# Kernel tuning notes

Hardware: AMD Instinct MI355X
Metric: run time of the kernel (lower is better)

The kernel has to match this reference:

```python
import jax, jax.numpy as jnp
import numpy as np

B, LQ, D, H, NL, NP, DFF = 8, 1800, 256, 8, 4, 4, 1024
DH = D // H
SHAPES = np.array([[100, 150], [50, 75], [25, 38], [13, 19]], dtype=np.int64)
LIN = int((SHAPES[:, 0] * SHAPES[:, 1]).sum())
QN, QP = -8.0, 7.0  # 4-bit signed LSQ


def lsq(w, alpha):
    """LSQ weight quantization (per-tensor scale, STE round/grad-scale)."""
    g = 1.0 / jnp.sqrt(w.size * QP)
    a = alpha * g + jax.lax.stop_gradient(alpha - alpha * g)  # grad-scaled alpha
    wn = jnp.clip(w / a, QN, QP)
    wq = wn + jax.lax.stop_gradient(jnp.round(wn) - wn)       # round with STE
    return wq * a


def linear_q(x, w, b, a):
    return x @ lsq(w, a).T + b


def layer_norm(x, g, b, eps=1e-5):
    m = x.mean(-1, keepdims=True)
    v = ((x - m) ** 2).mean(-1, keepdims=True)
    return (x - m) / jnp.sqrt(v + eps) * g + b


def setup_inputs():
    key = jax.random.key(0)
    ks = list(jax.random.split(key, 20))

    def nrm(i, shape, s=0.02):
        return jax.random.normal(ks[i], shape, jnp.float32) * s

    def alpha(w):
        return 2.0 * jnp.mean(jnp.abs(w)) / jnp.sqrt(QP)

    qW, kW, vW, oW = nrm(0, (D, D)), nrm(1, (D, D)), nrm(2, (D, D)), nrm(3, (D, D))
    val_W = nrm(4, (D, D))
    off_W = nrm(5, (H * NL * NP * 2, D))
    aw_W = nrm(6, (H * NL * NP, D))
    out_W = nrm(7, (D, D))
    W1, W2 = nrm(8, (DFF, D)), nrm(9, (D, DFF))
    lsi = np.concatenate([[0], np.cumsum(SHAPES[:, 0] * SHAPES[:, 1])[:-1]]).astype(np.int64)
    z = jnp.zeros
    return dict(
        tgt=nrm(10, (B, LQ, D), 1.0),
        query_pos=nrm(11, (B, LQ, D), 1.0),
        reference_points=jax.random.uniform(ks[12], (B, LQ, NL, 2), jnp.float32),
        src=nrm(13, (B, LIN, D), 1.0),
        qW=qW, qb=z(D), kW=kW, kb=z(D), vW=vW, vb=z(D), oW=oW, ob=z(D),
        a_q=alpha(qW), a_k=alpha(kW), a_v=alpha(vW), a_o=alpha(oW),
        val_W=val_W, val_b=z(D), a_val=alpha(val_W),
        off_W=off_W, off_b=z(H * NL * NP * 2),
        aw_W=aw_W, aw_b=z(H * NL * NP),
        out_W=out_W, out_b=z(D), a_out=alpha(out_W),
        W1=W1, b1=z(DFF), a_w1=alpha(W1),
        W2=W2, b2=z(D), a_w2=alpha(W2),
        ln1_g=jnp.ones(D), ln1_b=z(D),
        ln2_g=jnp.ones(D), ln2_b=z(D),
        ln3_g=jnp.ones(D), ln3_b=z(D),
        src_spatial_shapes=jnp.asarray(SHAPES),
        level_start_index=jnp.asarray(lsi),
        src_padding_mask=jnp.zeros((B, LIN), dtype=bool),
    )


def reference(tgt, query_pos, reference_points, src,
              qW, qb, kW, kb, vW, vb, oW, ob, a_q, a_k, a_v, a_o,
              val_W, val_b, a_val, off_W, off_b, aw_W, aw_b, out_W, out_b, a_out,
              W1, b1, a_w1, W2, b2, a_w2,
              ln1_g, ln1_b, ln2_g, ln2_b, ln3_g, ln3_b,
              src_spatial_shapes, level_start_index, src_padding_mask):
    shapes = np.asarray(src_spatial_shapes)  # static spatial shapes per level

    # ---- quantized self-attention (dropout = eval mode, i.e. identity) ----
    qk_in = tgt + query_pos
    q = linear_q(qk_in, qW, qb, a_q).reshape(B, LQ, H, DH)
    k = linear_q(qk_in, kW, kb, a_k).reshape(B, LQ, H, DH)
    v = linear_q(tgt, vW, vb, a_v).reshape(B, LQ, H, DH)
    scores = jnp.einsum('bqhd,bkhd->bhqk', q, k) / jnp.sqrt(jnp.float32(DH))
    p = jax.nn.softmax(scores, axis=-1)
    sa = jnp.einsum('bhqk,bkhd->bqhd', p, v).reshape(B, LQ, D)
    tgt = layer_norm(tgt + linear_q(sa, oW, ob, a_o), ln2_g, ln2_b)

    # ---- quantized multi-scale deformable cross-attention ----
    query = tgt + query_pos
    value = linear_q(src, val_W, val_b, a_val)
    value = jnp.where(src_padding_mask[..., None], 0.0, value)
    value = value.reshape(B, LIN, H, DH)
    offs = (query @ off_W.T + off_b).reshape(B, LQ, H, NL, NP, 2)
    aw = (query @ aw_W.T + aw_b).reshape(B, LQ, H, NL * NP)
    aw = jax.nn.softmax(aw, axis=-1).reshape(B, LQ, H, NL, NP)
    # offset normalizer is (W_l, H_l)
    norm = jnp.asarray(shapes[:, ::-1].astype(np.float32))  # [NL, 2]
    loc = reference_points[:, :, None, :, None, :] + offs / norm[None, None, None, :, None, :]

    bidx = jnp.arange(B)[:, None, None, None]
    hidx = jnp.arange(H)[None, None, :, None]
    acc = jnp.zeros((B, LQ, H, DH), jnp.float32)
    start = 0
    for l in range(NL):
        Hl, Wl = int(shapes[l, 0]), int(shapes[l, 1])
        v_l = jax.lax.dynamic_slice_in_dim(value, start, Hl * Wl, 1).reshape(B, Hl, Wl, H, DH)
        # grid_sample semantics: align_corners=False, zero padding
        x = loc[:, :, :, l, :, 0] * Wl - 0.5  # [B, LQ, H, NP]
        y = loc[:, :, :, l, :, 1] * Hl - 0.5
        x0 = jnp.floor(x); y0 = jnp.floor(y)
        x0i = x0.astype(jnp.int32); y0i = y0.astype(jnp.int32)
        wx1 = x - x0; wy1 = y - y0
        wx0 = 1.0 - wx1; wy0 = 1.0 - wy1

        def gather(yi, xi):
            valid = (yi >= 0) & (yi < Hl) & (xi >= 0) & (xi < Wl)
            yc = jnp.clip(yi, 0, Hl - 1); xc = jnp.clip(xi, 0, Wl - 1)
            g = v_l[bidx, yc, xc, hidx]  # [B, LQ, H, NP, DH]
            return g * valid[..., None]

        samp = (gather(y0i, x0i) * (wy0 * wx0)[..., None]
                + gather(y0i, x0i + 1) * (wy0 * wx1)[..., None]
                + gather(y0i + 1, x0i) * (wy1 * wx0)[..., None]
                + gather(y0i + 1, x0i + 1) * (wy1 * wx1)[..., None])
        acc = acc + (aw[:, :, :, l, :, None] * samp).sum(axis=3)
        start += Hl * Wl

    ca = linear_q(acc.reshape(B, LQ, D), out_W, out_b, a_out)
    tgt = layer_norm(tgt + ca, ln1_g, ln1_b)

    # ---- quantized FFN ----
    t2 = linear_q(jax.nn.relu(linear_q(tgt, W1, b1, a_w1)), W2, b2, a_w2)
    tgt = layer_norm(tgt + t2, ln3_g, ln3_b)
    return tgt
```

## Files before the change

kernel.cpp:

```cpp
#include <hip/hip_runtime.h>
#include <hip/hip_bf16.h>

static constexpr int B_   = 8;
static constexpr int LQ_  = 1800;
static constexpr int D_   = 256;
static constexpr int H_   = 8;
static constexpr int DFF_ = 1024;
static constexpr int LIN_ = 19947;
static constexpr int MQ_  = B_ * LQ_;
static constexpr int NELEM_ = MQ_ * D_;

#define CDIV(a, b) (((a) + (b) - 1) / (b))

typedef unsigned short u16;
typedef unsigned int   u32;
typedef unsigned long long u64;
typedef __attribute__((ext_vector_type(8))) __bf16 bf16x8;
typedef __attribute__((ext_vector_type(4))) float  f32x4;
typedef __attribute__((ext_vector_type(4))) u32    u32x4;

#if __has_builtin(__builtin_amdgcn_exp2f)
#define EXP2(x) __builtin_amdgcn_exp2f(x)
#else
#define EXP2(x) exp2f(x)
#endif

__device__ __forceinline__ u16 f2bf(float f) {
    union { __bf16 h; u16 u; } v; v.h = (__bf16)f; return v.u;
}
__device__ __forceinline__ float bf2f(u16 u) {
    union { u32 u; float f; } v; v.u = ((u32)u) << 16;
    return v.f;
}

__device__ __forceinline__ f32x4 mfma_bf16(bf16x8 a, bf16x8 b, f32x4 c) {
    return __builtin_amdgcn_mfma_f32_16x16x32_bf16(a, b, c, 0, 0, 0);
}

__global__ void k_quant(const float* __restrict__ w, const float* __restrict__ alpha,
                        u16* __restrict__ o, int n) {
    int i = blockIdx.x * blockDim.x + threadIdx.x;
    if (i >= n) return;
    float a = alpha[0];
    float wn = fminf(fmaxf(w[i] / a, -8.f), 7.f);
    o[i] = f2bf(rintf(wn) * a);
}

__global__ void k_cvt(const float* __restrict__ w, u16* __restrict__ o, int n) {
    int i = blockIdx.x * blockDim.x + threadIdx.x;
    if (i < n) o[i] = f2bf(w[i]);
}

__global__ void k_addcvt(const float* __restrict__ a, const float* __restrict__ b,
                         u16* __restrict__ o, int n) {
    int i = blockIdx.x * blockDim.x + threadIdx.x;
    if (i < n) o[i] = f2bf(a[i] + b[i]);
}

__global__ void k_addcvt2(const u16* __restrict__ a, const float* __restrict__ b,
                          u16* __restrict__ o, int n) {
    int i = blockIdx.x * blockDim.x + threadIdx.x;
    if (i < n) o[i] = f2bf(bf2f(a[i]) + b[i]);
}

struct rawf8 { float4 a, b; };
__device__ __forceinline__ bf16x8 loadraw(const u16* p) { return *(const bf16x8*)p; }
__device__ __forceinline__ rawf8  loadraw(const float* p) {
    rawf8 r; r.a = *(const float4*)p; r.b = *(const float4*)(p + 4); return r;
}
__device__ __forceinline__ void wlds(u16* d, bf16x8 v) { *(bf16x8*)d = v; }
__device__ __forceinline__ void wlds(u16* d, rawf8 v) {
    bf16x8 r;
    r[0] = (__bf16)v.a.x; r[1] = (__bf16)v.a.y; r[2] = (__bf16)v.a.z; r[3] = (__bf16)v.a.w;
    r[4] = (__bf16)v.b.x; r[5] = (__bf16)v.b.y; r[6] = (__bf16)v.b.z; r[7] = (__bf16)v.b.w;
    *(bf16x8*)d = r;
}
__device__ __forceinline__ void storey(float* p, float v) { *p = v; }
__device__ __forceinline__ void storey(u16* p, float v)   { *p = f2bf(v); }

template <typename XT, typename OT, bool RELU>
__global__ __launch_bounds__(512) void k_gemm2(
    const XT* __restrict__ X, const u16* __restrict__ W,
    const float* __restrict__ bias, OT* __restrict__ Y,
    int M, int N, int K)
{
    __shared__ u16 As[2][128 * 40];
    __shared__ u16 Bs[2][256 * 40];
    const int tid = threadIdx.x;
    const int wave = tid >> 6, lane = tid & 63;
    const int wr = wave >> 2, wc = wave & 3;
    const int fr = lane & 15, fg = lane >> 4;
    const int bm = blockIdx.x * 128, bn = blockIdx.y * 256;

    const int xr = tid >> 2, xc = (tid & 3) * 8;
    const int wrow = tid >> 1, wcol = (tid & 1) * 16;

    int gr0 = bm + xr; if (gr0 > M - 1) gr0 = M - 1;
    const XT*  xp0 = X + (size_t)gr0 * K + xc;
    const u16* wp0 = W + (size_t)(bn + wrow) * K + wcol;

    f32x4 acc[4][4];
    #pragma unroll
    for (int m = 0; m < 4; ++m)
        #pragma unroll
        for (int n = 0; n < 4; ++n) acc[m][n] = (f32x4){0.f, 0.f, 0.f, 0.f};

    wlds(&As[0][xr * 40 + xc], loadraw(xp0));
    wlds(&Bs[0][wrow * 40 + wcol],     loadraw(wp0));
    wlds(&Bs[0][wrow * 40 + wcol + 8], loadraw(wp0 + 8));
    __syncthreads();

    const int nk = K >> 5;
    int cur = 0;
    for (int kt = 0; kt < nk; ++kt) {
        const bool nxt = (kt + 1 < nk);
        decltype(loadraw(xp0)) xa{};
        bf16x8 wb0{}, wb1{};
        if (nxt) {
            int k0 = (kt + 1) << 5;
            xa  = loadraw(xp0 + k0);
            wb0 = loadraw(wp0 + k0);
            wb1 = loadraw(wp0 + k0 + 8);
        }
        bf16x8 af[4], bg[4];
        #pragma unroll
        for (int m = 0; m < 4; ++m)
            af[m] = *(const bf16x8*)&As[cur][(wr * 64 + m * 16 + fr) * 40 + fg * 8];
        #pragma unroll
        for (int n = 0; n < 4; ++n)
            bg[n] = *(const bf16x8*)&Bs[cur][(wc * 64 + n * 16 + fr) * 40 + fg * 8];
        #pragma unroll
        for (int m = 0; m < 4; ++m)
            #pragma unroll
            for (int n = 0; n < 4; ++n)
                acc[m][n] = mfma_bf16(af[m], bg[n], acc[m][n]);
        if (nxt) {
            wlds(&As[cur ^ 1][xr * 40 + xc], xa);
            wlds(&Bs[cur ^ 1][wrow * 40 + wcol],     wb0);
            wlds(&Bs[cur ^ 1][wrow * 40 + wcol + 8], wb1);
            __syncthreads();
            cur ^= 1;
        }
    }

    #pragma unroll
    for (int m = 0; m < 4; ++m) {
        #pragma unroll
        for (int i = 0; i < 4; ++i) {
            int grow = bm + wr * 64 + m * 16 + fg * 4 + i;
            if (grow >= M) continue;
            #pragma unroll
            for (int n = 0; n < 4; ++n) {
                int gcol = bn + wc * 64 + n * 16 + fr;
                float v = acc[m][n][i] + bias[gcol];
                if (RELU) v = fmaxf(v, 0.f);
                storey(Y + (size_t)grow * N + gcol, v);
            }
        }
    }
}

__device__ __forceinline__ bf16x8 loadx(const u16* p) { return *(const bf16x8*)p; }
template <typename XT, typename OT, bool RELU>
__global__ __launch_bounds__(256) void k_gemm(
    const XT* __restrict__ X, const u16* __restrict__ W,
    const float* __restrict__ bias, OT* __restrict__ Y,
    int M, int N, int K)
{
    __shared__ u16 Ash[128 * 40];
    __shared__ u16 Bsh[128 * 40];
    const int tid = threadIdx.x;
    const int wave = tid >> 6, lane = tid & 63;
    const int wr = wave >> 1, wc = wave & 1;
    const int fr = lane & 15, fg = lane >> 4;
    const int bm = blockIdx.x * 128, bn = blockIdx.y * 128;
    const int srow = tid >> 2, sc = (tid & 3) * 8;

    f32x4 acc[4][4];
    #pragma unroll
    for (int m = 0; m < 4; ++m)
        #pragma unroll
        for (int n = 0; n < 4; ++n) acc[m][n] = (f32x4){0.f, 0.f, 0.f, 0.f};

    for (int k0 = 0; k0 < K; k0 += 32) {
        __syncthreads();
        #pragma unroll
        for (int i = 0; i < 2; ++i) {
            int row = srow + i * 64;
            int gr = bm + row; if (gr > M - 1) gr = M - 1;
            wlds(&Ash[row * 40 + sc], loadraw(X + (size_t)gr * K + k0 + sc));
            int wn = bn + row; if (wn > N - 1) wn = N - 1;
            wlds(&Bsh[row * 40 + sc], loadraw(W + (size_t)wn * K + k0 + sc));
        }
        __syncthreads();
        bf16x8 af[4], bg[4];
        #pragma unroll
        for (int m = 0; m < 4; ++m)
            af[m] = *(const bf16x8*)&Ash[(wr * 64 + m * 16 + fr) * 40 + fg * 8];
        #pragma unroll
        for (int n = 0; n < 4; ++n)
            bg[n] = *(const bf16x8*)&Bsh[(wc * 64 + n * 16 + fr) * 40 + fg * 8];
        #pragma unroll
        for (int m = 0; m < 4; ++m)
            #pragma unroll
            for (int n = 0; n < 4; ++n)
                acc[m][n] = mfma_bf16(af[m], bg[n], acc[m][n]);
    }

    #pragma unroll
    for (int m = 0; m < 4; ++m) {
        #pragma unroll
        for (int i = 0; i < 4; ++i) {
            int grow = bm + wr * 64 + m * 16 + fg * 4 + i;
            if (grow >= M) continue;
            #pragma unroll
            for (int n = 0; n < 4; ++n) {
                int gcol = bn + wc * 64 + n * 16 + fr;
                if (gcol >= N) continue;
                float v = acc[m][n][i] + bias[gcol];
                if (RELU) v = fmaxf(v, 0.f);
                storey(Y + (size_t)grow * N + gcol, v);
            }
        }
    }
}

__global__ __launch_bounds__(256) void k_attn(
    const u16* __restrict__ Q, const u16* __restrict__ K,
    const u16* __restrict__ V, u16* __restrict__ O)
{
    __shared__ u16 Ks[128 * 40];
    __shared__ u16 Vt[32 * 136];
    const int b = blockIdx.z, h = blockIdx.y;
    const int q0 = blockIdx.x * 64;
    const int tid = threadIdx.x;
    const int wave = tid >> 6, lane = tid & 63;
    const int fr = lane & 15, fg = lane >> 4;
    constexpr float C2 = 0.25503486f;

    int qg = q0 + wave * 16 + fr; if (qg >= LQ_) qg = LQ_ - 1;
    bf16x8 qf;
    {
        bf16x8 qraw = *(const bf16x8*)&Q[((size_t)(b * LQ_ + qg)) * 256 + h * 32 + fg * 8];
        #pragma unroll
        for (int j = 0; j < 8; ++j) qf[j] = (__bf16)((float)qraw[j] * C2);
    }

    const bf16x8 ones = {(__bf16)1.f, (__bf16)1.f, (__bf16)1.f, (__bf16)1.f,
                         (__bf16)1.f, (__bf16)1.f, (__bf16)1.f, (__bf16)1.f};

    f32x4 o0 = (f32x4){0.f,0.f,0.f,0.f}, o1 = (f32x4){0.f,0.f,0.f,0.f};
    f32x4 lacc = (f32x4){0.f,0.f,0.f,0.f};

    const int kr = tid >> 1, kc = (tid & 1) * 16;
    const int vp = lane, vdh = wave * 8;
    const int cp = ((vp >> 4) << 4) | (((vp >> 1) & 3) << 2) | (((vp >> 3) & 1) << 1) | (vp & 1);

    for (int kb0 = 0; kb0 < LQ_; kb0 += 128) {
        const bool tail = (kb0 + 128 > LQ_);
        __syncthreads();
        {
            int kg = kb0 + kr; if (kg >= LQ_) kg = LQ_ - 1;
            const u16* kp = &K[((size_t)(b * LQ_ + kg)) * 256 + h * 32 + kc];
            *(bf16x8*)&Ks[kr * 40 + kc]     = *(const bf16x8*)kp;
            *(bf16x8*)&Ks[kr * 40 + kc + 8] = *(const bf16x8*)(kp + 8);
            int v0 = kb0 + 2 * vp, v1 = v0 + 1;
            if (v0 >= LQ_) v0 = LQ_ - 1;
            if (v1 >= LQ_) v1 = LQ_ - 1;
            union { bf16x8 v; u16 s[8]; } va, vb2;
            va.v  = *(const bf16x8*)&V[((size_t)(b * LQ_ + v0)) * 256 + h * 32 + vdh];
            vb2.v = *(const bf16x8*)&V[((size_t)(b * LQ_ + v1)) * 256 + h * 32 + vdh];
            #pragma unroll
            for (int j = 0; j < 8; ++j)
                *(u32*)&Vt[(vdh + j) * 136 + 2 * cp] = (u32)va.s[j] | ((u32)vb2.s[j] << 16);
        }
        __syncthreads();

        u32x4 pq[4];
        #pragma unroll
        for (int f = 0; f < 8; ++f) {
            bf16x8 ka = *(const bf16x8*)&Ks[(f * 16 + fr) * 40 + fg * 8];
            f32x4 s = mfma_bf16(ka, qf, (f32x4){0.f,0.f,0.f,0.f});
            if (tail) {
                #pragma unroll
                for (int i = 0; i < 4; ++i)
                    if (kb0 + f * 16 + fg * 4 + i >= LQ_) s[i] = -3e38f;
            }
            float p0 = EXP2(s[0]), p1 = EXP2(s[1]);
            float p2 = EXP2(s[2]), p3 = EXP2(s[3]);
            union { __bf16 h[2]; u32 w; } c0, c1;
            c0.h[0] = (__bf16)p0; c0.h[1] = (__bf16)p1;
            c1.h[0] = (__bf16)p2; c1.h[1] = (__bf16)p3;
            pq[f >> 1][(f & 1) * 2 + 0] = c0.w;
            pq[f >> 1][(f & 1) * 2 + 1] = c1.w;
        }

        #pragma unroll
        for (int ks = 0; ks < 4; ++ks) {
            bf16x8 pb  = __builtin_bit_cast(bf16x8, pq[ks]);
            bf16x8 va0 = *(const bf16x8*)&Vt[fr * 136 + ks * 32 + fg * 8];
            bf16x8 va1 = *(const bf16x8*)&Vt[(16 + fr) * 136 + ks * 32 + fg * 8];
            o0 = mfma_bf16(va0, pb, o0);
            o1 = mfma_bf16(va1, pb, o1);
            lacc = mfma_bf16(ones, pb, lacc);
        }
    }

    float inv = 1.f / lacc[0];
    int qout = q0 + wave * 16 + fr;
    if (qout < LQ_) {
        size_t base = ((size_t)(b * LQ_ + qout)) * 256 + h * 32;
        #pragma unroll
        for (int i = 0; i < 4; ++i) {
            O[base + fg * 4 + i]      = f2bf(o0[i] * inv);
            O[base + 16 + fg * 4 + i] = f2bf(o1[i] * inv);
        }
    }
}

__device__ __forceinline__ float ldf(const float* p) { return *p; }
__device__ __forceinline__ float ldf(const u16* p)   { return bf2f(*p); }

template <typename RT, typename OT>
__global__ __launch_bounds__(256) void k_resln(
    const u16* __restrict__ X, const RT* __restrict__ R,
    const float* __restrict__ g, const float* __restrict__ bb,
    OT* __restrict__ O)
{
    const int row = blockIdx.x;
    const int d = threadIdx.x;
    const size_t off = (size_t)row * D_ + d;
    float v = ldf(R + off) + bf2f(X[off]);
    __shared__ float r1[4], r2[4];
    int lane = d & 63, wid = d >> 6;
    float s = v;
    #pragma unroll
    for (int o_ = 32; o_ >= 1; o_ >>= 1) s += __shfl_xor(s, o_);
    if (lane == 0) r1[wid] = s;
    __syncthreads();
    float mean = (r1[0] + r1[1] + r1[2] + r1[3]) * (1.f / 256.f);
    float dv = v - mean;
    float sq = dv * dv;
    #pragma unroll
    for (int o_ = 32; o_ >= 1; o_ >>= 1) sq += __shfl_xor(sq, o_);
    if (lane == 0) r2[wid] = sq;
    __syncthreads();
    float var = (r2[0] + r2[1] + r2[2] + r2[3]) * (1.f / 256.f);
    storey(O + off, dv / sqrtf(var + 1e-5f) * g[d] + bb[d]);
}

__global__ __launch_bounds__(256) void k_sample(
    const float* __restrict__ offs, const float* __restrict__ aw,
    const u16* __restrict__ value, const float* __restrict__ refp,
    u16* __restrict__ acc_out)
{
    __shared__ u32 pts[2][128][8];
    const int t = threadIdx.x;
    const int bq0 = blockIdx.x * 2;
    const int b = bq0 / LQ_;

    constexpr int Hl[4] = {100, 50, 25, 13};
    constexpr int Wl[4] = {150, 75, 38, 19};
    constexpr int LS[4] = {0, 15000, 18750, 19700};

    {
        const int qsub = t >> 7;
        const int pt = t & 127;
        const int h = pt >> 4, lp = pt & 15;
        const int l = lp >> 2, p = lp & 3;
        const int bq = bq0 + qsub;

        float2 oxy = *(const float2*)&offs[(size_t)bq * 256 + h * 32 + l * 8 + p * 2];
        float av = aw[(size_t)bq * 128 + h * 16 + lp];
        float mx = av;
        #pragma unroll
        for (int s = 1; s < 16; s <<= 1) mx = fmaxf(mx, __shfl_xor(mx, s));
        float e = __expf(av - mx);
        float sum = e;
        #pragma unroll
        for (int s = 1; s < 16; s <<= 1) sum += __shfl_xor(sum, s);
        float a = e / sum;

        float2 rxy = *(const float2*)&refp[(size_t)bq * 8 + l * 2];
        const float Wf = (float)Wl[l], Hf = (float)Hl[l];
        float x = (rxy.x + oxy.x / Wf) * Wf - 0.5f;
        float y = (rxy.y + oxy.y / Hf) * Hf - 0.5f;
        float x0f = floorf(x), y0f = floorf(y);
        int x0 = (int)x0f, y0 = (int)y0f;
        float wx1 = x - x0f, wy1 = y - y0f;
        float wx0 = 1.f - wx1, wy0 = 1.f - wy1;

        u32 ov[4]; float wv[4];
        #pragma unroll
        for (int c = 0; c < 4; ++c) {
            int cy = c >> 1, cx = c & 1;
            int yi = y0 + cy, xi = x0 + cx;
            bool valid = (yi >= 0) && (yi < Hl[l]) && (xi >= 0) && (xi < Wl[l]);
            ov[c] = valid ? (u32)((LS[l] + yi * Wl[l] + xi) * 256 + h * 32) : 0u;
            float w = (cy ? wy1 : wy0) * (cx ? wx1 : wx0) * a;
            wv[c] = valid ? w : 0.f;
        }
        u32* dst = pts[qsub][lp * 8 + h];
        *(uint4*)dst = make_uint4(ov[0], ov[1], ov[2], ov[3]);
        float4 wq = make_float4(wv[0], wv[1], wv[2], wv[3]);
        *(float4*)(dst + 4) = wq;
    }
    __syncthreads();

    const int qsub = t >> 7;
    const int h = (t >> 4) & 7;
    const int dp = t & 15;
    const u16* vb = value + (size_t)b * LIN_ * 256 + 2 * dp;
    float a0 = 0.f, a1 = 0.f;
    #pragma unroll
    for (int i = 0; i < 16; ++i) {
        const u32* P = pts[qsub][i * 8 + h];
        uint4 o4 = *(const uint4*)P;
        float4 w4 = *(const float4*)(P + 4);
        u32 g;
        g = *(const u32*)&vb[o4.x]; a0 += w4.x * bf2f((u16)g); a1 += w4.x * bf2f((u16)(g >> 16));
        g = *(const u32*)&vb[o4.y]; a0 += w4.y * bf2f((u16)g); a1 += w4.y * bf2f((u16)(g >> 16));
        g = *(const u32*)&vb[o4.z]; a0 += w4.z * bf2f((u16)g); a1 += w4.z * bf2f((u16)(g >> 16));
        g = *(const u32*)&vb[o4.w]; a0 += w4.w * bf2f((u16)g); a1 += w4.w * bf2f((u16)(g >> 16));
    }
    const int bq = bq0 + qsub;
    u32 packed = (u32)f2bf(a0) | ((u32)f2bf(a1) << 16);
    *(u32*)&acc_out[(size_t)bq * 256 + h * 32 + 2 * dp] = packed;
}

extern "C" void kernel_launch(void* const* d_in, const int* in_sizes, int n_in,
                              void* d_out, int out_size, void* d_ws, size_t ws_size,
                              hipStream_t stream)
{
    (void)in_sizes; (void)n_in; (void)out_size; (void)ws_size;
    const float* tgt   = (const float*)d_in[0];
    const float* qpos  = (const float*)d_in[1];
    const float* refp  = (const float*)d_in[2];
    const float* src   = (const float*)d_in[3];
    const float* qW    = (const float*)d_in[4];
    const float* qb    = (const float*)d_in[5];
    const float* kW    = (const float*)d_in[6];
    const float* kb    = (const float*)d_in[7];
    const float* vW    = (const float*)d_in[8];
    const float* vb    = (const float*)d_in[9];
    const float* oW    = (const float*)d_in[10];
    const float* ob    = (const float*)d_in[11];
    const float* a_q   = (const float*)d_in[12];
    const float* a_k   = (const float*)d_in[13];
    const float* a_v   = (const float*)d_in[14];
    const float* a_o   = (const float*)d_in[15];
    const float* val_W = (const float*)d_in[16];
    const float* val_b = (const float*)d_in[17];
    const float* a_val = (const float*)d_in[18];
    const float* off_W = (const float*)d_in[19];
    const float* off_b = (const float*)d_in[20];
    const float* aw_W  = (const float*)d_in[21];
    const float* aw_b  = (const float*)d_in[22];
    const float* out_W = (const float*)d_in[23];
    const float* out_b = (const float*)d_in[24];
    const float* a_out = (const float*)d_in[25];
    const float* W1    = (const float*)d_in[26];
    const float* b1    = (const float*)d_in[27];
    const float* a_w1  = (const float*)d_in[28];
    const float* W2    = (const float*)d_in[29];
    const float* b2    = (const float*)d_in[30];
    const float* a_w2  = (const float*)d_in[31];
    const float* ln1_g = (const float*)d_in[32];
    const float* ln1_b = (const float*)d_in[33];
    const float* ln2_g = (const float*)d_in[34];
    const float* ln2_b = (const float*)d_in[35];
    const float* ln3_g = (const float*)d_in[36];
    const float* ln3_b = (const float*)d_in[37];

    u16* wq_q  = (u16*)d_ws;
    u16* wq_k  = wq_q + 65536;
    u16* wq_v  = wq_k + 65536;
    u16* wq_o  = wq_v + 65536;
    u16* wq_vl = wq_o + 65536;
    u16* wq_ot = wq_vl + 65536;
    u16* w_off = wq_ot + 65536;
    u16* w_aw  = w_off + 65536;
    u16* wq_1  = w_aw + 32768;
    u16* wq_2  = wq_1 + 262144;
    u16* bufA  = wq_2 + 262144;
    u16* bufB  = bufA + NELEM_;
    u16* bufC  = bufB + NELEM_;
    u16* bufD  = bufC + NELEM_;
    u16* bufE  = bufD + NELEM_;
    float* offs = (float*)(bufE + NELEM_);
    float* awb  = offs + NELEM_;
    u16* valb   = (u16*)(awb + MQ_ * 128);

    const int TB = 256;
    const int MVAL = B_ * LIN_;
    const int GX = CDIV(MQ_, 128);

    k_quant<<<CDIV(65536, TB), TB, 0, stream>>>(qW, a_q, wq_q, 65536);
    k_quant<<<CDIV(65536, TB), TB, 0, stream>>>(kW, a_k, wq_k, 65536);
    k_quant<<<CDIV(65536, TB), TB, 0, stream>>>(vW, a_v, wq_v, 65536);
    k_quant<<<CDIV(65536, TB), TB, 0, stream>>>(oW, a_o, wq_o, 65536);
    k_quant<<<CDIV(65536, TB), TB, 0, stream>>>(val_W, a_val, wq_vl, 65536);
    k_quant<<<CDIV(65536, TB), TB, 0, stream>>>(out_W, a_out, wq_ot, 65536);
    k_quant<<<CDIV(262144, TB), TB, 0, stream>>>(W1, a_w1, wq_1, 262144);
    k_quant<<<CDIV(262144, TB), TB, 0, stream>>>(W2, a_w2, wq_2, 262144);
    k_cvt<<<CDIV(65536, TB), TB, 0, stream>>>(off_W, w_off, 65536);
    k_cvt<<<CDIV(32768, TB), TB, 0, stream>>>(aw_W, w_aw, 32768);

    k_addcvt<<<CDIV(NELEM_, TB), TB, 0, stream>>>(tgt, qpos, bufA, NELEM_);
    k_cvt<<<CDIV(NELEM_, TB), TB, 0, stream>>>(tgt, bufB, NELEM_);

    k_gemm2<u16, u16, false><<<dim3(GX, 1), 512, 0, stream>>>(bufA, wq_q, qb, bufC, MQ_, 256, 256);
    k_gemm2<u16, u16, false><<<dim3(GX, 1), 512, 0, stream>>>(bufA, wq_k, kb, bufD, MQ_, 256, 256);
    k_gemm2<u16, u16, false><<<dim3(GX, 1), 512, 0, stream>>>(bufB, wq_v, vb, bufE, MQ_, 256, 256);
    k_attn<<<dim3(CDIV(LQ_,64), H_, B_), TB, 0, stream>>>(bufC, bufD, bufE, bufA);
    k_gemm2<u16, u16, false><<<dim3(GX, 1), 512, 0, stream>>>(bufA, wq_o, ob, bufB, MQ_, 256, 256);
    k_resln<float, u16><<<MQ_, TB, 0, stream>>>(bufB, tgt, ln2_g, ln2_b, bufC);

    k_addcvt2<<<CDIV(NELEM_, TB), TB, 0, stream>>>(bufC, qpos, bufD, NELEM_);
    k_gemm2<float, u16, false><<<dim3(CDIV(MVAL,128), 1), 512, 0, stream>>>(src, wq_vl, val_b, valb, MVAL, 256, 256);
    k_gemm2<u16, float, false><<<dim3(GX, 1), 512, 0, stream>>>(bufD, w_off, off_b, offs, MQ_, 256, 256);
    k_gemm<u16, float, false><<<dim3(GX, 1), TB, 0, stream>>>(bufD, w_aw, aw_b, awb, MQ_, 128, 256);
    k_sample<<<MQ_ / 2, TB, 0, stream>>>(offs, awb, valb, refp, bufE);
    k_gemm2<u16, u16, false><<<dim3(GX, 1), 512, 0, stream>>>(bufE, wq_ot, out_b, bufA, MQ_, 256, 256);
    k_resln<u16, u16><<<MQ_, TB, 0, stream>>>(bufA, bufC, ln1_g, ln1_b, bufB);

    u16* ffn1 = valb;
    k_gemm2<u16, u16, true ><<<dim3(GX, 4), 512, 0, stream>>>(bufB, wq_1, b1, ffn1, MQ_, 1024, 256);
    k_gemm2<u16, u16, false><<<dim3(GX, 1), 512, 0, stream>>>(ffn1, wq_2, b2, bufD, MQ_, 256, 1024);
    k_resln<u16, float><<<MQ_, TB, 0, stream>>>(bufD, bufB, ln3_g, ln3_b, (float*)d_out);
}
```

Baseline: 398.6 us.

## Replace GEMM with direct global-to-LDS loads, XOR-swizzled LDS and smaller tiles

Replaces the 512-thread 128x256 GEMM with a 256-thread kernel using 64xBN tiles. Operand tiles are staged into LDS with the global_load_lds builtin, which skips the register round trip, and an XOR swizzle on the unpadded 32-wide rows avoids bank conflicts. Smaller tiles give more blocks for the M=14400 GEMMs, which matters on a GPU with many CUs. The cost is more redundant weight loads per output. For the fp32 src input, the conversion to bf16 now happens after the LDS read.

```diff
diff --git a/kernel.cpp b/kernel.cpp
--- a/kernel.cpp
+++ b/kernel.cpp
@@ -37,6 +37,13 @@
     return __builtin_amdgcn_mfma_f32_16x16x32_bf16(a, b, c, 0, 0, 0);
 }
 
+__device__ __forceinline__ void gload16(const void* g, void* l) {
+    __builtin_amdgcn_global_load_lds(
+        (const __attribute__((address_space(1))) void*)g,
+        (__attribute__((address_space(3))) void*)l,
+        16, 0, 0);
+}
+
 __global__ void k_quant(const float* __restrict__ w, const float* __restrict__ alpha,
                         u16* __restrict__ o, int n) {
     int i = blockIdx.x * blockDim.x + threadIdx.x;
@@ -78,80 +85,111 @@
 __device__ __forceinline__ void storey(float* p, float v) { *p = v; }
 __device__ __forceinline__ void storey(u16* p, float v)   { *p = f2bf(v); }
 
-template <typename XT, typename OT, bool RELU>
-__global__ __launch_bounds__(512) void k_gemm2(
+template <typename XT, typename OT, bool RELU, int BN>
+__global__ __launch_bounds__(256) void k_gemm3(
     const XT* __restrict__ X, const u16* __restrict__ W,
     const float* __restrict__ bias, OT* __restrict__ Y,
     int M, int N, int K)
 {
-    __shared__ u16 As[2][128 * 40];
-    __shared__ u16 Bs[2][256 * 40];
+    constexpr int WN  = BN / 2;
+    constexpr int NFR = WN / 16;
+    constexpr bool XF32 = (sizeof(XT) == 4);
+    constexpr int ASZ = 64 * 32 * (XF32 ? 2 : 1);
+    constexpr int BSZ = BN * 32;
+    __shared__ __align__(16) u16 As[2][ASZ];
+    __shared__ __align__(16) u16 Bs[2][BSZ];
+
     const int tid = threadIdx.x;
     const int wave = tid >> 6, lane = tid & 63;
-    const int wr = wave >> 2, wc = wave & 3;
+    const int wr = wave >> 1, wc = wave & 1;
     const int fr = lane & 15, fg = lane >> 4;
-    const int bm = blockIdx.x * 128, bn = blockIdx.y * 256;
-
-    const int xr = tid >> 2, xc = (tid & 3) * 8;
-    const int wrow = tid >> 1, wcol = (tid & 1) * 16;
-
-    int gr0 = bm + xr; if (gr0 > M - 1) gr0 = M - 1;
-    const XT*  xp0 = X + (size_t)gr0 * K + xc;
-    const u16* wp0 = W + (size_t)(bn + wrow) * K + wcol;
-
-    f32x4 acc[4][4];
-    #pragma unroll
-    for (int m = 0; m < 4; ++m)
-        #pragma unroll
-        for (int n = 0; n < 4; ++n) acc[m][n] = (f32x4){0.f, 0.f, 0.f, 0.f};
-
-    wlds(&As[0][xr * 40 + xc], loadraw(xp0));
-    wlds(&Bs[0][wrow * 40 + wcol],     loadraw(wp0));
-    wlds(&Bs[0][wrow * 40 + wcol + 8], loadraw(wp0 + 8));
+    const int bm = blockIdx.x * 64, bn = blockIdx.y * BN;
+
+    f32x4 acc[2][NFR];
+    #pragma unroll
+    for (int m = 0; m < 2; ++m)
+        #pragma unroll
+        for (int n = 0; n < NFR; ++n) acc[m][n] = (f32x4){0.f, 0.f, 0.f, 0.f};
+
+    auto stageA = [&](int buf, int kt) {
+        if constexpr (!XF32) {
+            int r = (wave << 4) + (lane >> 2);
+            int grow = bm + r; if (grow > M - 1) grow = M - 1;
+            int cs = (lane & 3) ^ ((lane >> 3) & 3);
+            gload16((const u16*)X + (size_t)grow * K + (kt << 5) + (cs << 3),
+                    &As[buf][wave * 512]);
+        } else {
+            float* Af = (float*)As[buf];
+            #pragma unroll
+            for (int t = 0; t < 2; ++t) {
+                int r = (t << 5) + (wave << 3) + (lane >> 3);
+                int grow = bm + r; if (grow > M - 1) grow = M - 1;
+                int cs = (lane & 7) ^ ((lane >> 3) & 7);
+                gload16((const float*)X + (size_t)grow * K + (kt << 5) + (cs << 2),
+                        &Af[((t << 5) + (wave << 3)) * 32]);
+            }
+        }
+    };
+    auto stageB = [&](int buf, int kt) {
+        #pragma unroll
+        for (int t = 0; t < BN / 64; ++t) {
+            int r = (t << 6) + (wave << 4) + (lane >> 2);
+            int cs = (lane & 3) ^ ((lane >> 3) & 3);
+            gload16(W + (size_t)(bn + r) * K + (kt << 5) + (cs << 3),
+                    &Bs[buf][((t << 6) + (wave << 4)) * 32]);
+        }
+    };
+
+    stageA(0, 0); stageB(0, 0);
     __syncthreads();
 
     const int nk = K >> 5;
     int cur = 0;
     for (int kt = 0; kt < nk; ++kt) {
-        const bool nxt = (kt + 1 < nk);
-        decltype(loadraw(xp0)) xa{};
-        bf16x8 wb0{}, wb1{};
-        if (nxt) {
-            int k0 = (kt + 1) << 5;
-            xa  = loadraw(xp0 + k0);
-            wb0 = loadraw(wp0 + k0);
-            wb1 = loadraw(wp0 + k0 + 8);
-        }
-        bf16x8 af[4], bg[4];
-        #pragma unroll
-        for (int m = 0; m < 4; ++m)
-            af[m] = *(const bf16x8*)&As[cur][(wr * 64 + m * 16 + fr) * 40 + fg * 8];
-        #pragma unroll
-        for (int n = 0; n < 4; ++n)
-            bg[n] = *(const bf16x8*)&Bs[cur][(wc * 64 + n * 16 + fr) * 40 + fg * 8];
-        #pragma unroll
-        for (int m = 0; m < 4; ++m)
+        if (kt + 1 < nk) { stageA(cur ^ 1, kt + 1); stageB(cur ^ 1, kt + 1); }
+
+        bf16x8 af[2], bg[NFR];
+        #pragma unroll
+        for (int m = 0; m < 2; ++m) {
+            int r = wr * 32 + m * 16 + fr;
+            if constexpr (!XF32) {
+                af[m] = *(const bf16x8*)&As[cur][r * 32 + ((fg ^ ((fr >> 1) & 3)) << 3)];
+            } else {
+                const float* Af = (const float*)As[cur];
+                int s0 = (fg << 1) ^ (fr & 7);
+                f32x4 x0 = *(const f32x4*)&Af[r * 32 + (s0 << 2)];
+                f32x4 x1 = *(const f32x4*)&Af[r * 32 + ((s0 ^ 1) << 2)];
+                #pragma unroll
+                for (int j = 0; j < 4; ++j) {
+                    af[m][j]     = (__bf16)x0[j];
+                    af[m][4 + j] = (__bf16)x1[j];
+                }
+            }
+        }
+        #pragma unroll
+        for (int n = 0; n < NFR; ++n) {
+            int r = wc * WN + n * 16 + fr;
+            bg[n] = *(const bf16x8*)&Bs[cur][r * 32 + ((fg ^ ((fr >> 1) & 3)) << 3)];
+        }
+        #pragma unroll
+        for (int m = 0; m < 2; ++m)
             #pragma unroll
-            for (int n = 0; n < 4; ++n)
+            for (int n = 0; n < NFR; ++n)
                 acc[m][n] = mfma_bf16(af[m], bg[n], acc[m][n]);
-        if (nxt) {
-            wlds(&As[cur ^ 1][xr * 40 + xc], xa);
-            wlds(&Bs[cur ^ 1][wrow * 40 + wcol],     wb0);
-            wlds(&Bs[cur ^ 1][wrow * 40 + wcol + 8], wb1);
-            __syncthreads();
-            cur ^= 1;
-        }
-    }
-
-    #pragma unroll
-    for (int m = 0; m < 4; ++m) {
+
+        __syncthreads();
+        cur ^= 1;
+    }
+
+    #pragma unroll
+    for (int m = 0; m < 2; ++m) {
         #pragma unroll
         for (int i = 0; i < 4; ++i) {
-            int grow = bm + wr * 64 + m * 16 + fg * 4 + i;
+            int grow = bm + wr * 32 + m * 16 + fg * 4 + i;
             if (grow >= M) continue;
             #pragma unroll
-            for (int n = 0; n < 4; ++n) {
-                int gcol = bn + wc * 64 + n * 16 + fr;
+            for (int n = 0; n < NFR; ++n) {
+                int gcol = bn + wc * WN + n * 16 + fr;
                 float v = acc[m][n][i] + bias[gcol];
                 if (RELU) v = fmaxf(v, 0.f);
                 storey(Y + (size_t)grow * N + gcol, v);
@@ -160,7 +198,6 @@
     }
 }
 
-__device__ __forceinline__ bf16x8 loadx(const u16* p) { return *(const bf16x8*)p; }
 template <typename XT, typename OT, bool RELU>
 __global__ __launch_bounds__(256) void k_gemm(
     const XT* __restrict__ X, const u16* __restrict__ W,
@@ -493,7 +530,8 @@
 
     const int TB = 256;
     const int MVAL = B_ * LIN_;
-    const int GX = CDIV(MQ_, 128);
+    const int GM = MQ_ / 64;
+    const int GV = CDIV(MVAL, 64);
 
     k_quant<<<CDIV(65536, TB), TB, 0, stream>>>(qW, a_q, wq_q, 65536);
     k_quant<<<CDIV(65536, TB), TB, 0, stream>>>(kW, a_k, wq_k, 65536);
@@ -509,23 +547,23 @@
     k_addcvt<<<CDIV(NELEM_, TB), TB, 0, stream>>>(tgt, qpos, bufA, NELEM_);
     k_cvt<<<CDIV(NELEM_, TB), TB, 0, stream>>>(tgt, bufB, NELEM_);
 
-    k_gemm2<u16, u16, false><<<dim3(GX, 1), 512, 0, stream>>>(bufA, wq_q, qb, bufC, MQ_, 256, 256);
-    k_gemm2<u16, u16, false><<<dim3(GX, 1), 512, 0, stream>>>(bufA, wq_k, kb, bufD, MQ_, 256, 256);
-    k_gemm2<u16, u16, false><<<dim3(GX, 1), 512, 0, stream>>>(bufB, wq_v, vb, bufE, MQ_, 256, 256);
+    k_gemm3<u16, u16, false, 128><<<dim3(GM, 2), TB, 0, stream>>>(bufA, wq_q, qb, bufC, MQ_, 256, 256);
+    k_gemm3<u16, u16, false, 128><<<dim3(GM, 2), TB, 0, stream>>>(bufA, wq_k, kb, bufD, MQ_, 256, 256);
+    k_gemm3<u16, u16, false, 128><<<dim3(GM, 2), TB, 0, stream>>>(bufB, wq_v, vb, bufE, MQ_, 256, 256);
     k_attn<<<dim3(CDIV(LQ_,64), H_, B_), TB, 0, stream>>>(bufC, bufD, bufE, bufA);
-    k_gemm2<u16, u16, false><<<dim3(GX, 1), 512, 0, stream>>>(bufA, wq_o, ob, bufB, MQ_, 256, 256);
+    k_gemm3<u16, u16, false, 128><<<dim3(GM, 2), TB, 0, stream>>>(bufA, wq_o, ob, bufB, MQ_, 256, 256);
     k_resln<float, u16><<<MQ_, TB, 0, stream>>>(bufB, tgt, ln2_g, ln2_b, bufC);
 
     k_addcvt2<<<CDIV(NELEM_, TB), TB, 0, stream>>>(bufC, qpos, bufD, NELEM_);
-    k_gemm2<float, u16, false><<<dim3(CDIV(MVAL,128), 1), 512, 0, stream>>>(src, wq_vl, val_b, valb, MVAL, 256, 256);
-    k_gemm2<u16, float, false><<<dim3(GX, 1), 512, 0, stream>>>(bufD, w_off, off_b, offs, MQ_, 256, 256);
-    k_gemm<u16, float, false><<<dim3(GX, 1), TB, 0, stream>>>(bufD, w_aw, aw_b, awb, MQ_, 128, 256);
+    k_gemm3<float, u16, false, 256><<<dim3(GV, 1), TB, 0, stream>>>(src, wq_vl, val_b, valb, MVAL, 256, 256);
+    k_gemm3<u16, float, false, 128><<<dim3(GM, 2), TB, 0, stream>>>(bufD, w_off, off_b, offs, MQ_, 256, 256);
+    k_gemm<u16, float, false><<<dim3(CDIV(MQ_,128), 1), TB, 0, stream>>>(bufD, w_aw, aw_b, awb, MQ_, 128, 256);
     k_sample<<<MQ_ / 2, TB, 0, stream>>>(offs, awb, valb, refp, bufE);
-    k_gemm2<u16, u16, false><<<dim3(GX, 1), 512, 0, stream>>>(bufE, wq_ot, out_b, bufA, MQ_, 256, 256);
+    k_gemm3<u16, u16, false, 128><<<dim3(GM, 2), TB, 0, stream>>>(bufE, wq_ot, out_b, bufA, MQ_, 256, 256);
     k_resln<u16, u16><<<MQ_, TB, 0, stream>>>(bufA, bufC, ln1_g, ln1_b, bufB);
 
     u16* ffn1 = valb;
-    k_gemm2<u16, u16, true ><<<dim3(GX, 4), 512, 0, stream>>>(bufB, wq_1, b1, ffn1, MQ_, 1024, 256);
-    k_gemm2<u16, u16, false><<<dim3(GX, 1), 512, 0, stream>>>(ffn1, wq_2, b2, bufD, MQ_, 256, 1024);
+    k_gemm3<u16, u16, true , 128><<<dim3(GM, 8), TB, 0, stream>>>(bufB, wq_1, b1, ffn1, MQ_, 1024, 256);
+    k_gemm3<u16, u16, false, 128><<<dim3(GM, 2), TB, 0, stream>>>(ffn1, wq_2, b2, bufD, MQ_, 256, 1024);
     k_resln<u16, float><<<MQ_, TB, 0, stream>>>(bufD, bufB, ln3_g, ln3_b, (float*)d_out);
 }
```

After: 385.3 us. 3.3% less time.
